# Optimization experiments

Hardware: AMD Instinct MI355X
Metric: run time of the kernel (lower is better)

Reference implementation:

```python
import jax, jax.numpy as jnp
import numpy as np

DIM = 512; HEADS = 8; DHEAD = 64; INNER = HEADS * DHEAD
T = 9; H = 16; W = 16; KS = 5; KT = 7
SEQ = T * H * W + 1          # 2305 tokens incl. BOS
GH = 48; GW = 48             # axial grid: sqrt(T*H*W) = 48
B = 2


def _nearby_mask_np():
    """Faithful numpy port of generate_nearby_mask(causal=True). True = masked."""
    te = (KT - 1) // 2
    frame = H * W
    S = T * frame
    pad = KS // 2
    tmpl = (np.arange(KS * KS) >= (KS * KS) // 2).reshape(KS, KS)
    mb = np.ones((S, T, H + 2 * pad, W + 2 * pad), dtype=bool)
    for t in range(T):
        for h in range(H):
            for w in range(W):
                i = t * frame + h * W + w
                mb[i, t, h:h + KS, w:w + KS] = tmpl
                mb[i, max(0, t - te):t, h:h + KS, w:w + KS] = False
    mb = mb[:, :, pad:-pad, pad:-pad].reshape(S, S)
    mb = np.roll(mb, -1, axis=0)
    out = np.ones((S + 1, S + 1), dtype=bool)  # pad 1 row/col of True at top-left
    out[1:, 1:] = mb
    out[0, 0] = False
    return out


def setup_inputs() -> dict:
    key = jax.random.key(0)
    ks = jax.random.split(key, 16)
    inp = {
        "x": jax.random.normal(ks[0], (B, SEQ, DIM), jnp.float32),
        "nearby_mask": jnp.asarray(_nearby_mask_np()),
    }
    i = 1
    for l in range(3):
        for nm in ("Wq", "Wk", "Wv", "Wo"):
            inp[f"{nm}{l}"] = jax.random.normal(ks[i], (DIM, INNER), jnp.float32) * 0.02
            i += 1
        inp[f"bo{l}"] = jnp.zeros((DIM,), jnp.float32)
    return inp


def _neg(dt):
    return -jnp.finfo(dt).max


def _axial(x, Wq, Wk, Wv, Wo, bo, typ):
    # type 0: attend along rows (width axis); type 1: attend along columns.
    b = x.shape[0]
    scale = DHEAD ** -0.5
    q, k, v = x @ Wq, x @ Wk, x @ Wv

    def split(t):
        bos = t[:, :1].reshape(b, 1, HEADS, DHEAD).transpose(0, 2, 1, 3)[:, :, None]  # b hd 1 1 d
        img = t[:, 1:].reshape(b, GH, GW, HEADS, DHEAD)
        if typ == 0:
            img = img.transpose(0, 3, 1, 2, 4)  # b hd h w d
            nq = GH
        else:
            img = img.transpose(0, 3, 2, 1, 4)  # b hd w h d
            nq = GW
        bos = jnp.broadcast_to(bos, (b, HEADS, nq, 1, DHEAD))
        return jnp.concatenate([bos, img], axis=3)  # b hd nq (1+len) d

    qs, ks, vs = split(q), split(k), split(v)
    dots = jnp.einsum('bhnid,bhnjd->bhnij', qs, ks) * scale
    L = dots.shape[-1]
    causal = jnp.triu(jnp.ones((L, L), dtype=bool), 1)
    dots = jnp.where(causal, _neg(dots.dtype), dots)
    attn = jax.nn.softmax(dots, axis=-1)
    out = jnp.einsum('bhnij,bhnjd->bhnid', attn, vs)
    out_bos = out[:, :, 0, 0].reshape(b, 1, INNER)
    oi = out[:, :, :, 1:, :]
    if typ == 0:
        oi = oi.transpose(0, 2, 3, 1, 4).reshape(b, GH * GW, INNER)  # b (h w) (hd d)
    else:
        oi = oi.transpose(0, 3, 2, 1, 4).reshape(b, GH * GW, INNER)
    return jnp.concatenate([out_bos, oi], axis=1) @ Wo + bo


def _nearby(x, Wq, Wk, Wv, Wo, bo, mask):
    b, n, _ = x.shape
    scale = DHEAD ** -0.5
    q = (x @ Wq).reshape(b, n, HEADS, DHEAD).transpose(0, 2, 1, 3)
    k = (x @ Wk).reshape(b, n, HEADS, DHEAD).transpose(0, 2, 1, 3)
    v = (x @ Wv).reshape(b, n, HEADS, DHEAD).transpose(0, 2, 1, 3)
    dots = jnp.einsum('bhid,bhjd->bhij', q, k) * scale
    dots = jnp.where(mask, _neg(dots.dtype), dots)
    attn = jax.nn.softmax(dots, axis=-1)
    out = jnp.einsum('bhij,bhjd->bhid', attn, v)
    return out.transpose(0, 2, 1, 3).reshape(b, n, INNER) @ Wo + bo


def reference(x, nearby_mask,
              Wq0, Wk0, Wv0, Wo0, bo0,
              Wq1, Wk1, Wv1, Wo1, bo1,
              Wq2, Wk2, Wv2, Wo2, bo2):
    x = x + _axial(x, Wq0, Wk0, Wv0, Wo0, bo0, 0)   # row axial
    x = x + _axial(x, Wq1, Wk1, Wv1, Wo1, bo1, 1)   # column axial
    x = x + _nearby(x, Wq2, Wk2, Wv2, Wo2, bo2, nearby_mask)  # nearby sparse-mask attn
    return x
```

## Files before the change

kernel.cpp:

```cpp
#include <hip/hip_runtime.h>
#include <hip/hip_bf16.h>

#define SEQ 2305
#define NROWS 4610
#define MPAD 4736
#define DIM 512
#define QKVN 1536

typedef __attribute__((ext_vector_type(8))) short v8s;
typedef __attribute__((ext_vector_type(4))) float v4f;

__device__ __forceinline__ float bf2f(unsigned short u) {
    return __uint_as_float(((unsigned)u) << 16);
}

__device__ __forceinline__ void load_lds16(const void* g, void* l) {
    __builtin_amdgcn_global_load_lds(
        (const __attribute__((address_space(1))) void*)g,
        (__attribute__((address_space(3))) void*)l, 16, 0, 0);
}

struct WPack { const float* p[12]; };

__global__ void prep_inputs(WPack wp, __hip_bfloat16* __restrict__ wqkv,
                            __hip_bfloat16* __restrict__ wo,
                            const float4* __restrict__ xin, float4* __restrict__ xout,
                            __hip_bfloat16* __restrict__ xb, int n4) {
    int tx = threadIdx.x, ty = threadIdx.y;
    int m = blockIdx.z;
    if (m == 12) {
        int tidl = ty * 32 + tx;
        int bid = blockIdx.y * 16 + blockIdx.x;
        for (int i = bid * 256 + tidl; i < n4; i += 65536) {
            float4 v = xin[i];
            xout[i] = v;
            int j = i * 4;
            xb[j + 0] = __float2bfloat16(v.x);
            xb[j + 1] = __float2bfloat16(v.y);
            xb[j + 2] = __float2bfloat16(v.z);
            xb[j + 3] = __float2bfloat16(v.w);
        }
        return;
    }
    __shared__ float tile[32][33];
    const float* src = wp.p[m];
    int l = m >> 2, j = m & 3;
    __hip_bfloat16* dst = (j < 3) ? (wqkv + (size_t)l * QKVN * DIM + (size_t)j * DIM * DIM)
                                  : (wo + (size_t)l * DIM * DIM);
    int bx = blockIdx.x * 32, by = blockIdx.y * 32;
    #pragma unroll
    for (int i = 0; i < 4; i++)
        tile[ty + 8 * i][tx] = src[(size_t)(by + ty + 8 * i) * DIM + bx + tx];
    __syncthreads();
    #pragma unroll
    for (int i = 0; i < 4; i++)
        dst[(size_t)(bx + ty + 8 * i) * DIM + by + tx] = __float2bfloat16(tile[tx][ty + 8 * i]);
}

__global__ __launch_bounds__(256) void gemm_lds(
    const __hip_bfloat16* __restrict__ A, const __hip_bfloat16* __restrict__ Bt,
    float* __restrict__ C, const float* __restrict__ bias, const float* __restrict__ res,
    __hip_bfloat16* __restrict__ Cb, int M, int N) {
    __shared__ short As[2][64 * 32];
    __shared__ short Bs[2][128 * 32];
    const int K = 512;
    int tid = threadIdx.x;
    int wid = tid >> 6, lane = tid & 63;
    int quad = lane >> 4, l16 = lane & 15;
    int bM = blockIdx.x * 64, bN = blockIdx.y * 128;
    int wM = (wid >> 1) * 32, wN = (wid & 1) * 64;

    const short* Ag = (const short*)A;
    const short* Bg = (const short*)Bt;

    int rowS = tid >> 2, cg = tid & 3;
    const short* gA = Ag + (size_t)(bM + rowS) * K + cg * 8;
    const short* gB0 = Bg + (size_t)(bN + rowS) * K + cg * 8;
    const short* gB1 = Bg + (size_t)(bN + 64 + rowS) * K + cg * 8;

    v4f acc[2][4] = {};
    for (int k0 = 0; k0 < K; k0 += 64) {
        #pragma unroll
        for (int s = 0; s < 2; s++) {
            load_lds16(gA + k0 + s * 32, As[s] + wid * 512);
            load_lds16(gB0 + k0 + s * 32, Bs[s] + wid * 512);
            load_lds16(gB1 + k0 + s * 32, Bs[s] + 2048 + wid * 512);
        }
        __syncthreads();
        #pragma unroll
        for (int s = 0; s < 2; s++) {
            v8s af[2], bf[4];
            #pragma unroll
            for (int i = 0; i < 2; i++)
                af[i] = *(const v8s*)(As[s] + (wM + i * 16 + l16) * 32 + quad * 8);
            #pragma unroll
            for (int j = 0; j < 4; j++)
                bf[j] = *(const v8s*)(Bs[s] + (wN + j * 16 + l16) * 32 + quad * 8);
            #pragma unroll
            for (int i = 0; i < 2; i++)
                #pragma unroll
                for (int j = 0; j < 4; j++)
                    acc[i][j] = __builtin_amdgcn_mfma_f32_16x16x32_bf16(af[i], bf[j], acc[i][j], 0, 0, 0);
        }
        __syncthreads();
    }

    #pragma unroll
    for (int i = 0; i < 2; i++) {
        int row = bM + wM + i * 16 + quad * 4;
        #pragma unroll
        for (int j = 0; j < 4; j++) {
            int col = bN + wN + j * 16 + l16;
            #pragma unroll
            for (int r = 0; r < 4; r++) {
                int rr = row + r;
                if (rr < M) {
                    float v = acc[i][j][r];
                    if (bias) v += bias[col];
                    if (res) v += res[(size_t)rr * N + col];
                    size_t idx = (size_t)rr * N + col;
                    if (C) C[idx] = v;
                    if (Cb) Cb[idx] = __float2bfloat16(v);
                }
            }
        }
    }
}

__global__ __launch_bounds__(256) void axial_flash(
    const unsigned short* __restrict__ qkvb, __hip_bfloat16* __restrict__ attn_b, int typ) {
    __shared__ short Ks[64 * 64];
    __shared__ short Vs[64 * 64];
    __shared__ short Ps[64 * 72];
    __shared__ float invl[64];

    int tid = threadIdx.x;
    int wid = tid >> 6, lane = tid & 63;
    int quad = lane >> 4, l16 = lane & 15;
    int n = blockIdx.x;
    int b = blockIdx.y >> 3, h = blockIdx.y & 7;
    size_t rowbase = (size_t)b * SEQ;
    int hoff = h * 64;

    #pragma unroll
    for (int it = 0; it < 2; it++) {
        int linear = it * 256 + tid;
        int slot = linear >> 3;
        int cd = linear & 7;
        int cs = cd ^ (slot & 7);
        int sp = (slot == 0) ? 0
               : (slot <= 48 ? (typ == 0 ? 1 + n * 48 + (slot - 1) : 1 + (slot - 1) * 48 + n) : 0);
        const unsigned short* srcK = qkvb + (rowbase + sp) * QKVN + hoff + 512 + cs * 8;
        load_lds16(srcK, Ks + it * 2048 + wid * 512 + lane * 8);
        const unsigned short* srcV = qkvb + (rowbase + sp) * QKVN + hoff + 1024 + cd * 8;
        load_lds16(srcV, Vs + it * 2048 + wid * 512 + lane * 8);
    }

    int qi = wid * 16 + l16;
    int sp_q = (qi >= 1 && qi <= 48)
             ? (typ == 0 ? 1 + n * 48 + (qi - 1) : 1 + (qi - 1) * 48 + n) : 0;
    const unsigned short* qptr = qkvb + (rowbase + sp_q) * QKVN + hoff + quad * 8;
    v8s qa0 = *(const v8s*)qptr;
    v8s qa1 = *(const v8s*)(qptr + 32);

    __syncthreads();

    if (n == 0 && tid < 64) {
        attn_b[rowbase * DIM + hoff + tid] =
            __float2bfloat16(bf2f(qkvb[rowbase * QKVN + hoff + 1024 + tid]));
    }

    v4f st[4];
    #pragma unroll
    for (int kt = 0; kt < 4; kt++) {
        int slot = kt * 16 + l16;
        int s7 = slot & 7;
        v8s blo = *(const v8s*)(Ks + slot * 64 + ((quad ^ s7) * 8));
        v8s bhi = *(const v8s*)(Ks + slot * 64 + (((4 + quad) ^ s7) * 8));
        v4f a = {};
        a = __builtin_amdgcn_mfma_f32_16x16x32_bf16(qa0, blo, a, 0, 0, 0);
        a = __builtin_amdgcn_mfma_f32_16x16x32_bf16(qa1, bhi, a, 0, 0, 0);
        st[kt] = a;
    }

    const float NEG = -3.0e38f;
    float sv[4][4];
    float pm[4] = {NEG, NEG, NEG, NEG};
    #pragma unroll
    for (int kt = 0; kt < 4; kt++) {
        int j = kt * 16 + l16;
        #pragma unroll
        for (int r = 0; r < 4; r++) {
            int i = wid * 16 + quad * 4 + r;
            bool ok = (i >= 1) && (i <= 48) && (j <= i);
            float v = ok ? st[kt][r] * 0.125f : NEG;
            sv[kt][r] = v;
            pm[r] = fmaxf(pm[r], v);
        }
    }
    #pragma unroll
    for (int r = 0; r < 4; r++)
        for (int o = 1; o < 16; o <<= 1) pm[r] = fmaxf(pm[r], __shfl_xor(pm[r], o));

    float ps[4] = {0.f, 0.f, 0.f, 0.f};
    #pragma unroll
    for (int kt = 0; kt < 4; kt++) {
        int j = kt * 16 + l16;
        #pragma unroll
        for (int r = 0; r < 4; r++) {
            float e = __expf(sv[kt][r] - pm[r]);
            ps[r] += e;
            Ps[(wid * 16 + quad * 4 + r) * 72 + j] = (short)__bfloat16_as_ushort(__float2bfloat16(e));
        }
    }
    #pragma unroll
    for (int r = 0; r < 4; r++)
        for (int o = 1; o < 16; o <<= 1) ps[r] += __shfl_xor(ps[r], o);
    if (l16 == 0) {
        #pragma unroll
        for (int r = 0; r < 4; r++)
            invl[wid * 16 + quad * 4 + r] = 1.0f / ps[r];
    }
    __syncthreads();

    #pragma unroll
    for (int qt = 0; qt < 4; qt++) {
        v4f oc = {};
        #pragma unroll
        for (int kc = 0; kc < 2; kc++) {
            v8s pa = *(const v8s*)(Ps + (qt * 16 + l16) * 72 + kc * 32 + quad * 8);
            v8s bfr;
            #pragma unroll
            for (int jj = 0; jj < 8; jj++)
                bfr[jj] = Vs[(kc * 32 + quad * 8 + jj) * 64 + wid * 16 + l16];
            oc = __builtin_amdgcn_mfma_f32_16x16x32_bf16(pa, bfr, oc, 0, 0, 0);
        }
        #pragma unroll
        for (int r = 0; r < 4; r++) {
            int i = qt * 16 + quad * 4 + r;
            if (i >= 1 && i <= 48) {
                int sp = typ == 0 ? 1 + n * 48 + (i - 1) : 1 + (i - 1) * 48 + n;
                attn_b[(rowbase + sp) * DIM + hoff + wid * 16 + l16] =
                    __float2bfloat16(oc[r] * invl[i]);
            }
        }
    }
}

__global__ __launch_bounds__(256) void nearby_flash(
    const unsigned short* __restrict__ qkvb, __hip_bfloat16* __restrict__ attn_b) {
    __shared__ short KV[256 * 64];
    __shared__ __hip_bfloat16 Ps[16 * 264];
    __shared__ float redm[16 * 4];
    __shared__ float reds[16 * 4];

    int tid = threadIdx.x;
    int wid = tid >> 6, lane = tid & 63;
    int quad = lane >> 4, l16 = lane & 15;

    int idx = blockIdx.x;
    if (idx >= 2304) {
        int bh = idx - 2304;
        int b = bh >> 3, h = bh & 7;
        size_t rb = (size_t)b * SEQ;
        const unsigned short* vb = qkvb + rb * QKVN + h * 64 + 1024 + lane;
        float s0 = 0.f, s1 = 0.f, s2 = 0.f, s3 = 0.f;
        int j = wid;
        for (; j + 12 < SEQ; j += 16) {
            s0 += bf2f(vb[(size_t)j * QKVN]);
            s1 += bf2f(vb[(size_t)(j + 4) * QKVN]);
            s2 += bf2f(vb[(size_t)(j + 8) * QKVN]);
            s3 += bf2f(vb[(size_t)(j + 12) * QKVN]);
        }
        for (; j < SEQ; j += 4) s0 += bf2f(vb[(size_t)j * QKVN]);
        float* red = (float*)KV;
        red[wid * 64 + lane] = s0 + s1 + s2 + s3;
        __syncthreads();
        if (wid == 0) {
            float tot = red[lane] + red[64 + lane] + red[128 + lane] + red[192 + lane];
            attn_b[(rb + 2304) * DIM + h * 64 + lane] = __float2bfloat16(tot * (1.0f / 2305.0f));
            attn_b[rb * DIM + h * 64 + lane] = __float2bfloat16(bf2f(vb[0]));
        }
        return;
    }

    int bh = idx & 15;
    int tile = idx >> 4;
    int b = bh >> 3, h = bh & 7;
    int t = tile >> 4;
    int sxy = tile & 15;
    int hh0 = (sxy >> 2) * 4, ww0 = (sxy & 3) * 4;
    int nf = (t < 3 ? t : 3) + 1;
    int t0 = t - (nf - 1);

    size_t rowbase = (size_t)b * SEQ;
    int hoff = h * 64;

    #pragma unroll
    for (int it = 0; it < 8; it++) {
        int linear = it * 256 + tid;
        int slot = linear >> 3;
        int cd = linear & 7;
        int cs = cd ^ (slot & 7);
        int f = slot >> 6, uy = (slot >> 3) & 7, ux = slot & 7;
        int kh = hh0 - 2 + uy, kw = ww0 - 2 + ux;
        int kt = t0 + f;
        bool ok = (kh >= 0) && (kh < 16) && (kw >= 0) && (kw < 16) && (f < nf);
        int kp = ok ? (kt * 256 + kh * 16 + kw + 1) : 0;
        const unsigned short* src = qkvb + (rowbase + kp) * QKVN + hoff + 512 + cs * 8;
        load_lds16(src, KV + it * 2048 + wid * 512 + lane * 8);
    }

    int qp_f = t * 256 + (hh0 + (l16 >> 2)) * 16 + (ww0 + (l16 & 3));
    const unsigned short* qptr = qkvb + (rowbase + qp_f) * QKVN + hoff + quad * 8;
    v8s qa0 = *(const v8s*)qptr;
    v8s qa1 = *(const v8s*)(qptr + 32);

    __syncthreads();

    v4f st[4];
    #pragma unroll
    for (int k = 0; k < 4; k++) {
        int slot = (wid * 4 + k) * 16 + l16;
        int s7 = slot & 7;
        v8s blo = *(const v8s*)(KV + slot * 64 + ((quad ^ s7) * 8));
        v8s bhi = *(const v8s*)(KV + slot * 64 + (((4 + quad) ^ s7) * 8));
        v4f a = {};
        a = __builtin_amdgcn_mfma_f32_16x16x32_bf16(qa0, blo, a, 0, 0, 0);
        a = __builtin_amdgcn_mfma_f32_16x16x32_bf16(qa1, bhi, a, 0, 0, 0);
        st[k] = a;
    }

    const float NEG = -3.0e38f;
    float sv[4][4];
    float pm[4] = {NEG, NEG, NEG, NEG};
    #pragma unroll
    for (int k = 0; k < 4; k++) {
        int slot = (wid * 4 + k) * 16 + l16;
        int f = slot >> 6, uy = (slot >> 3) & 7, ux = slot & 7;
        int kh = hh0 - 2 + uy, kw = ww0 - 2 + ux;
        bool okb = (kh >= 0) && (kh < 16) && (kw >= 0) && (kw < 16) && (f < nf);
        int dyp2 = uy - quad;
        bool oky = okb && (dyp2 >= 0) && (dyp2 <= 4);
        #pragma unroll
        for (int r = 0; r < 4; r++) {
            int dxp2 = ux - r;
            bool ok = oky && (dxp2 >= 0) && (dxp2 <= 4);
            if (f == nf - 1) ok = ok && (dyp2 * 5 + dxp2 < 12);
            float v = ok ? st[k][r] * 0.125f : NEG;
            sv[k][r] = v;
            pm[r] = fmaxf(pm[r], v);
        }
    }
    #pragma unroll
    for (int r = 0; r < 4; r++)
        for (int o = 1; o < 16; o <<= 1) pm[r] = fmaxf(pm[r], __shfl_xor(pm[r], o));
    if (l16 == 0) {
        #pragma unroll
        for (int r = 0; r < 4; r++) redm[(quad * 4 + r) * 4 + wid] = pm[r];
    }
    __syncthreads();

    #pragma unroll
    for (int it = 0; it < 8; it++) {
        int linear = it * 256 + tid;
        int slot = linear >> 3;
        int cd = linear & 7;
        int f = slot >> 6, uy = (slot >> 3) & 7, ux = slot & 7;
        int kh = hh0 - 2 + uy, kw = ww0 - 2 + ux;
        int kt = t0 + f;
        bool ok = (kh >= 0) && (kh < 16) && (kw >= 0) && (kw < 16) && (f < nf);
        int kp = ok ? (kt * 256 + kh * 16 + kw + 1) : 0;
        const unsigned short* src = qkvb + (rowbase + kp) * QKVN + hoff + 1024 + cd * 8;
        load_lds16(src, KV + it * 2048 + wid * 512 + lane * 8);
    }

    float rm[4];
    #pragma unroll
    for (int r = 0; r < 4; r++) {
        int row = (quad * 4 + r) * 4;
        rm[r] = fmaxf(fmaxf(redm[row], redm[row + 1]), fmaxf(redm[row + 2], redm[row + 3]));
    }

    float ps[4] = {0.f, 0.f, 0.f, 0.f};
    #pragma unroll
    for (int k = 0; k < 4; k++) {
        int slot = (wid * 4 + k) * 16 + l16;
        #pragma unroll
        for (int r = 0; r < 4; r++) {
            float e = __expf(sv[k][r] - rm[r]);
            ps[r] += e;
            Ps[(quad * 4 + r) * 264 + slot] = __float2bfloat16(e);
        }
    }
    #pragma unroll
    for (int r = 0; r < 4; r++)
        for (int o = 1; o < 16; o <<= 1) ps[r] += __shfl_xor(ps[r], o);
    if (l16 == 0) {
        #pragma unroll
        for (int r = 0; r < 4; r++) reds[(quad * 4 + r) * 4 + wid] = ps[r];
    }
    __syncthreads();

    float inv[4];
    #pragma unroll
    for (int r = 0; r < 4; r++) {
        int row = (quad * 4 + r) * 4;
        float d = reds[row] + reds[row + 1] + reds[row + 2] + reds[row + 3];
        inv[r] = 1.0f / d;
    }

    v4f oc = {};
    #pragma unroll
    for (int kc = 0; kc < 8; kc++) {
        v8s pa = *(const v8s*)((const short*)Ps + l16 * 264 + kc * 32 + quad * 8);
        v8s bf;
        #pragma unroll
        for (int j = 0; j < 8; j++) {
            int slot = kc * 32 + quad * 8 + j;
            bf[j] = KV[slot * 64 + wid * 16 + l16];
        }
        oc = __builtin_amdgcn_mfma_f32_16x16x32_bf16(pa, bf, oc, 0, 0, 0);
    }

    #pragma unroll
    for (int r = 0; r < 4; r++) {
        int qp = t * 256 + (hh0 + quad) * 16 + (ww0 + r);
        if (qp != 0) {
            attn_b[(rowbase + qp) * DIM + hoff + wid * 16 + l16] =
                __float2bfloat16(oc[r] * inv[r]);
        }
    }
}

extern "C" void kernel_launch(void* const* d_in, const int* in_sizes, int n_in,
                              void* d_out, int out_size, void* d_ws, size_t ws_size,
                              hipStream_t stream) {
    const float* x = (const float*)d_in[0];
    float* xcur = (float*)d_out;

    char* ws = (char*)d_ws;
    size_t off = 0;
    auto alloc = [&](size_t bytes) -> void* {
        void* p = ws + off;
        off = (off + bytes + 255) & ~(size_t)255;
        return p;
    };
    __hip_bfloat16* wqkv  = (__hip_bfloat16*)alloc((size_t)3 * QKVN * DIM * 2);
    __hip_bfloat16* wo    = (__hip_bfloat16*)alloc((size_t)3 * DIM * DIM * 2);
    __hip_bfloat16* xb    = (__hip_bfloat16*)alloc((size_t)MPAD * DIM * 2);
    __hip_bfloat16* attnb = (__hip_bfloat16*)alloc((size_t)MPAD * DIM * 2);
    __hip_bfloat16* qkvb  = (__hip_bfloat16*)alloc((size_t)NROWS * QKVN * 2);

    const int nElem = NROWS * DIM;
    const int n4 = nElem / 4;

    WPack wp;
    for (int l = 0; l < 3; l++)
        for (int j = 0; j < 4; j++)
            wp.p[l * 4 + j] = (const float*)d_in[2 + l * 5 + j];
    prep_inputs<<<dim3(16, 16, 13), dim3(32, 8), 0, stream>>>(
        wp, wqkv, wo, (const float4*)x, (float4*)xcur, xb, n4);

    for (int l = 0; l < 3; l++) {
        gemm_lds<<<dim3(MPAD / 64, QKVN / 128), 256, 0, stream>>>(
            xb, wqkv + (size_t)l * QKVN * DIM, nullptr, nullptr, nullptr, qkvb, NROWS, QKVN);
        if (l < 2) {
            axial_flash<<<dim3(48, 16), 256, 0, stream>>>((const unsigned short*)qkvb, attnb, l);
        } else {
            nearby_flash<<<2304 + 16, 256, 0, stream>>>((const unsigned short*)qkvb, attnb);
        }
        const float* bo = (const float*)d_in[6 + l * 5];
        gemm_lds<<<dim3(MPAD / 64, DIM / 128), 256, 0, stream>>>(
            attnb, wo + (size_t)l * DIM * DIM, xcur, bo, xcur, xb, NROWS, DIM);
    }
}
```

Baseline: 295.2 us.

## Load K into registers, halve V LDS buffer, split mean-V into separate kernels

The nearby attention kernel now loads K fragments straight from global memory into registers instead of staging them through LDS. V is staged in two halves through a 16 KB swizzled LDS buffer, and the V load is issued before the score computation so it overlaps with the MFMAs. The BOS/last-row mean-of-V work moves out of the 16 tail blocks of the flash kernel into a two-stage parallel reduction (partial sums, then fold). This lowers LDS use per block, which may allow more blocks per CU, and shortens the serial tail, at the cost of two extra launches and an added barrier-plus-reload step in the PV loop.

```diff
diff --git a/kernel.cpp b/kernel.cpp
--- a/kernel.cpp
+++ b/kernel.cpp
@@ -247,9 +247,33 @@
     }
 }
 
+__global__ void meanv_part(const unsigned short* __restrict__ qkvb, float* __restrict__ part) {
+    int b = blockIdx.x >> 4, ch = blockIdx.x & 15;
+    int col = blockIdx.y * 256 + threadIdx.x;
+    int j0 = ch * 145, j1 = j0 + 145;
+    if (j1 > SEQ) j1 = SEQ;
+    const unsigned short* p = qkvb + (size_t)b * SEQ * QKVN + 1024 + col;
+    float s = 0.f;
+    #pragma unroll 4
+    for (int j = j0; j < j1; j++) s += bf2f(p[(size_t)j * QKVN]);
+    part[((size_t)(b * 16 + ch)) * 512 + col] = s;
+}
+__global__ void meanv_fold(const float* __restrict__ part,
+                           const unsigned short* __restrict__ qkvb,
+                           __hip_bfloat16* __restrict__ attn_b) {
+    int b = blockIdx.x;
+    int col = blockIdx.y * 256 + threadIdx.x;
+    float s = 0.f;
+    #pragma unroll
+    for (int ch = 0; ch < 16; ch++) s += part[((size_t)(b * 16 + ch)) * 512 + col];
+    attn_b[((size_t)b * SEQ + 2304) * DIM + col] = __float2bfloat16(s * (1.0f / 2305.0f));
+    attn_b[((size_t)b * SEQ) * DIM + col] =
+        __float2bfloat16(bf2f(qkvb[(size_t)b * SEQ * QKVN + 1024 + col]));
+}
+
 __global__ __launch_bounds__(256) void nearby_flash(
     const unsigned short* __restrict__ qkvb, __hip_bfloat16* __restrict__ attn_b) {
-    __shared__ short KV[256 * 64];
+    __shared__ short Vs[128 * 64];
     __shared__ __hip_bfloat16 Ps[16 * 264];
     __shared__ float redm[16 * 4];
     __shared__ float reds[16 * 4];
@@ -259,31 +283,6 @@
     int quad = lane >> 4, l16 = lane & 15;
 
     int idx = blockIdx.x;
-    if (idx >= 2304) {
-        int bh = idx - 2304;
-        int b = bh >> 3, h = bh & 7;
-        size_t rb = (size_t)b * SEQ;
-        const unsigned short* vb = qkvb + rb * QKVN + h * 64 + 1024 + lane;
-        float s0 = 0.f, s1 = 0.f, s2 = 0.f, s3 = 0.f;
-        int j = wid;
-        for (; j + 12 < SEQ; j += 16) {
-            s0 += bf2f(vb[(size_t)j * QKVN]);
-            s1 += bf2f(vb[(size_t)(j + 4) * QKVN]);
-            s2 += bf2f(vb[(size_t)(j + 8) * QKVN]);
-            s3 += bf2f(vb[(size_t)(j + 12) * QKVN]);
-        }
-        for (; j < SEQ; j += 4) s0 += bf2f(vb[(size_t)j * QKVN]);
-        float* red = (float*)KV;
-        red[wid * 64 + lane] = s0 + s1 + s2 + s3;
-        __syncthreads();
-        if (wid == 0) {
-            float tot = red[lane] + red[64 + lane] + red[128 + lane] + red[192 + lane];
-            attn_b[(rb + 2304) * DIM + h * 64 + lane] = __float2bfloat16(tot * (1.0f / 2305.0f));
-            attn_b[rb * DIM + h * 64 + lane] = __float2bfloat16(bf2f(vb[0]));
-        }
-        return;
-    }
-
     int bh = idx & 15;
     int tile = idx >> 4;
     int b = bh >> 3, h = bh & 7;
@@ -292,42 +291,49 @@
     int hh0 = (sxy >> 2) * 4, ww0 = (sxy & 3) * 4;
     int nf = (t < 3 ? t : 3) + 1;
     int t0 = t - (nf - 1);
-
     size_t rowbase = (size_t)b * SEQ;
     int hoff = h * 64;
 
-    #pragma unroll
-    for (int it = 0; it < 8; it++) {
-        int linear = it * 256 + tid;
-        int slot = linear >> 3;
-        int cd = linear & 7;
-        int cs = cd ^ (slot & 7);
+    auto slot_kp = [&](int slot) -> int {
         int f = slot >> 6, uy = (slot >> 3) & 7, ux = slot & 7;
         int kh = hh0 - 2 + uy, kw = ww0 - 2 + ux;
         int kt = t0 + f;
         bool ok = (kh >= 0) && (kh < 16) && (kw >= 0) && (kw < 16) && (f < nf);
-        int kp = ok ? (kt * 256 + kh * 16 + kw + 1) : 0;
-        const unsigned short* src = qkvb + (rowbase + kp) * QKVN + hoff + 512 + cs * 8;
-        load_lds16(src, KV + it * 2048 + wid * 512 + lane * 8);
-    }
+        return ok ? (kt * 256 + kh * 16 + kw + 1) : 0;
+    };
 
     int qp_f = t * 256 + (hh0 + (l16 >> 2)) * 16 + (ww0 + (l16 & 3));
     const unsigned short* qptr = qkvb + (rowbase + qp_f) * QKVN + hoff + quad * 8;
     v8s qa0 = *(const v8s*)qptr;
     v8s qa1 = *(const v8s*)(qptr + 32);
 
-    __syncthreads();
-
-    v4f st[4];
+    v8s kb_lo[4], kb_hi[4];
     #pragma unroll
     for (int k = 0; k < 4; k++) {
         int slot = (wid * 4 + k) * 16 + l16;
-        int s7 = slot & 7;
-        v8s blo = *(const v8s*)(KV + slot * 64 + ((quad ^ s7) * 8));
-        v8s bhi = *(const v8s*)(KV + slot * 64 + (((4 + quad) ^ s7) * 8));
+        int kp = slot_kp(slot);
+        const unsigned short* kr = qkvb + (rowbase + kp) * QKVN + hoff + 512;
+        kb_lo[k] = *(const v8s*)(kr + quad * 8);
+        kb_hi[k] = *(const v8s*)(kr + 32 + quad * 8);
+    }
+
+    #pragma unroll
+    for (int it = 0; it < 4; it++) {
+        int linear = it * 256 + tid;
+        int slot = linear >> 3;
+        int cd = linear & 7;
+        int cs = cd ^ ((slot >> 3) & 7);
+        int kp = slot_kp(slot);
+        const unsigned short* src = qkvb + (rowbase + kp) * QKVN + hoff + 1024 + cs * 8;
+        load_lds16(src, Vs + it * 2048 + wid * 512 + lane * 8);
+    }
+
+    v4f st[4];
+    #pragma unroll
+    for (int k = 0; k < 4; k++) {
         v4f a = {};
-        a = __builtin_amdgcn_mfma_f32_16x16x32_bf16(qa0, blo, a, 0, 0, 0);
-        a = __builtin_amdgcn_mfma_f32_16x16x32_bf16(qa1, bhi, a, 0, 0, 0);
+        a = __builtin_amdgcn_mfma_f32_16x16x32_bf16(qa0, kb_lo[k], a, 0, 0, 0);
+        a = __builtin_amdgcn_mfma_f32_16x16x32_bf16(qa1, kb_hi[k], a, 0, 0, 0);
         st[k] = a;
     }
 
@@ -361,20 +367,6 @@
     }
     __syncthreads();
 
-    #pragma unroll
-    for (int it = 0; it < 8; it++) {
-        int linear = it * 256 + tid;
-        int slot = linear >> 3;
-        int cd = linear & 7;
-        int f = slot >> 6, uy = (slot >> 3) & 7, ux = slot & 7;
-        int kh = hh0 - 2 + uy, kw = ww0 - 2 + ux;
-        int kt = t0 + f;
-        bool ok = (kh >= 0) && (kh < 16) && (kw >= 0) && (kw < 16) && (f < nf);
-        int kp = ok ? (kt * 256 + kh * 16 + kw + 1) : 0;
-        const unsigned short* src = qkvb + (rowbase + kp) * QKVN + hoff + 1024 + cd * 8;
-        load_lds16(src, KV + it * 2048 + wid * 512 + lane * 8);
-    }
-
     float rm[4];
     #pragma unroll
     for (int r = 0; r < 4; r++) {
@@ -410,15 +402,44 @@
         inv[r] = 1.0f / d;
     }
 
+    int dcol = wid * 16 + l16;
+    int c_r = dcol >> 3, d7 = dcol & 7;
     v4f oc = {};
     #pragma unroll
-    for (int kc = 0; kc < 8; kc++) {
+    for (int kc = 0; kc < 4; kc++) {
         v8s pa = *(const v8s*)((const short*)Ps + l16 * 264 + kc * 32 + quad * 8);
         v8s bf;
         #pragma unroll
         for (int j = 0; j < 8; j++) {
             int slot = kc * 32 + quad * 8 + j;
-            bf[j] = KV[slot * 64 + wid * 16 + l16];
+            int key = (slot >> 3) & 7;
+            bf[j] = Vs[(slot & 127) * 64 + ((c_r ^ key) * 8) + d7];
+        }
+        oc = __builtin_amdgcn_mfma_f32_16x16x32_bf16(pa, bf, oc, 0, 0, 0);
+    }
+    __syncthreads();
+
+    #pragma unroll
+    for (int it = 0; it < 4; it++) {
+        int linear = 1024 + it * 256 + tid;
+        int slot = linear >> 3;
+        int cd = linear & 7;
+        int cs = cd ^ ((slot >> 3) & 7);
+        int kp = slot_kp(slot);
+        const unsigned short* src = qkvb + (rowbase + kp) * QKVN + hoff + 1024 + cs * 8;
+        load_lds16(src, Vs + it * 2048 + wid * 512 + lane * 8);
+    }
+    __syncthreads();
+
+    #pragma unroll
+    for (int kc = 4; kc < 8; kc++) {
+        v8s pa = *(const v8s*)((const short*)Ps + l16 * 264 + kc * 32 + quad * 8);
+        v8s bf;
+        #pragma unroll
+        for (int j = 0; j < 8; j++) {
+            int slot = kc * 32 + quad * 8 + j;
+            int key = (slot >> 3) & 7;
+            bf[j] = Vs[(slot & 127) * 64 + ((c_r ^ key) * 8) + d7];
         }
         oc = __builtin_amdgcn_mfma_f32_16x16x32_bf16(pa, bf, oc, 0, 0, 0);
     }
@@ -427,7 +448,7 @@
     for (int r = 0; r < 4; r++) {
         int qp = t * 256 + (hh0 + quad) * 16 + (ww0 + r);
         if (qp != 0) {
-            attn_b[(rowbase + qp) * DIM + hoff + wid * 16 + l16] =
+            attn_b[(rowbase + qp) * DIM + hoff + dcol] =
                 __float2bfloat16(oc[r] * inv[r]);
         }
     }
@@ -450,6 +471,7 @@
     __hip_bfloat16* wo    = (__hip_bfloat16*)alloc((size_t)3 * DIM * DIM * 2);
     __hip_bfloat16* xb    = (__hip_bfloat16*)alloc((size_t)MPAD * DIM * 2);
     __hip_bfloat16* attnb = (__hip_bfloat16*)alloc((size_t)MPAD * DIM * 2);
+    float* part           = (float*)alloc((size_t)2 * 16 * 512 * 4);
     __hip_bfloat16* qkvb  = (__hip_bfloat16*)alloc((size_t)NROWS * QKVN * 2);
 
     const int nElem = NROWS * DIM;
@@ -468,7 +490,9 @@
         if (l < 2) {
             axial_flash<<<dim3(48, 16), 256, 0, stream>>>((const unsigned short*)qkvb, attnb, l);
         } else {
-            nearby_flash<<<2304 + 16, 256, 0, stream>>>((const unsigned short*)qkvb, attnb);
+            meanv_part<<<dim3(32, 2), 256, 0, stream>>>((const unsigned short*)qkvb, part);
+            meanv_fold<<<dim3(2, 2), 256, 0, stream>>>(part, (const unsigned short*)qkvb, attnb);
+            nearby_flash<<<2304, 256, 0, stream>>>((const unsigned short*)qkvb, attnb);
         }
         const float* bo = (const float*)d_in[6 + l * 5];
         gemm_lds<<<dim3(MPAD / 64, DIM / 128), 256, 0, stream>>>(
```

After: 290.6 us. About the same (-1.6%).
